# Kernel optimization log

Hardware: AMD Instinct MI355X
Metric: run time of the kernel (lower is better)

The kernel has to match this reference:

```python
import jax, jax.numpy as jnp
import numpy as np

B, T, A, G, E, H = 64, 128, 30, 3, 64, 256
FA, FE, NE = 32, 16, 30
LA = A * 36
SD = A * FA + NE * FE + LA  # 2520


def setup_inputs() -> dict:
    key = jax.random.key(0)
    ks = iter(jax.random.split(key, 64))
    p = lambda *s: jax.random.normal(next(ks), s, jnp.float32) * 0.02
    qvals = jax.random.normal(next(ks), (B, T, A), jnp.float32)
    # ally states with a valid one-hot group type in the last G slots (constant over t)
    ally = jax.random.normal(next(ks), (B, T, A, FA), jnp.float32)
    grp = jax.random.randint(next(ks), (B, A), 0, G)
    onehot = jax.nn.one_hot(grp, G, dtype=jnp.float32)  # (B,A,G)
    ally = ally.at[:, :, :, -G:].set(jnp.broadcast_to(onehot[:, None], (B, T, A, G)))
    rest = jax.random.normal(next(ks), (B, T, NE * FE + LA), jnp.float32)
    states = jnp.concatenate([ally.reshape(B, T, A * FA), rest], axis=2)
    d = {"qvals": qvals, "states": states}
    d["g_w1_W1"] = p(G, SD, H); d["g_w1_b1"] = p(G, H); d["g_w1_W2"] = p(G, H, A * E); d["g_w1_b2"] = p(G, A * E)
    d["g_b1_W1"] = p(G, SD, H); d["g_b1_b1"] = p(G, H); d["g_b1_W2"] = p(G, H, E); d["g_b1_b2"] = p(G, E)
    d["g_w2_W1"] = p(G, SD, H); d["g_w2_b1"] = p(G, H); d["g_w2_W2"] = p(G, H, E); d["g_w2_b2"] = p(G, E)
    d["g_b2_W1"] = p(G, SD, E); d["g_b2_b1"] = p(G, E); d["g_b2_W2"] = p(G, E, 1); d["g_b2_b2"] = p(G, 1)
    d["h_w1_W1"] = p(SD, H); d["h_w1_b1"] = p(H); d["h_w1_W2"] = p(H, G * E); d["h_w1_b2"] = p(G * E)
    d["h_b1_W1"] = p(SD, H); d["h_b1_b1"] = p(H); d["h_b1_W2"] = p(H, E); d["h_b1_b2"] = p(E)
    d["h_w2_W1"] = p(SD, H); d["h_w2_b1"] = p(H); d["h_w2_W2"] = p(H, E); d["h_w2_b2"] = p(E)
    d["h_b2_W1"] = p(SD, E); d["h_b2_b1"] = p(E); d["h_b2_W2"] = p(E, 1); d["h_b2_b2"] = p(1)
    return d


def reference(qvals, states,
              g_w1_W1, g_w1_b1, g_w1_W2, g_w1_b2,
              g_b1_W1, g_b1_b1, g_b1_W2, g_b1_b2,
              g_w2_W1, g_w2_b1, g_w2_W2, g_w2_b2,
              g_b2_W1, g_b2_b1, g_b2_W2, g_b2_b2,
              h_w1_W1, h_w1_b1, h_w1_W2, h_w1_b2,
              h_b1_W1, h_b1_b1, h_b1_W2, h_b1_b2,
              h_w2_W1, h_w2_b1, h_w2_W2, h_w2_b2,
              h_b2_W1, h_b2_b1, h_b2_W2, h_b2_b2):
    N = B * T
    s = states.reshape(N, SD)
    # group masks from the one-hot type slots at t=0 (constant across time)
    ally = states[..., : A * FA].reshape(B, T, A, FA)
    type0 = ally[:, 0, :, -G:]                                  # (B,A,G)
    masks = jnp.transpose(type0 == 1.0, (2, 0, 1)).astype(qvals.dtype)  # (G,B,A)
    mq = (qvals[None] * masks[:, :, None, :]).reshape(G, N, A)  # (G,N,A)

    def gmlp(W1, b1, W2, b2):  # stacked-over-groups 2-layer MLP
        h = jax.nn.relu(jnp.einsum('nd,gdh->gnh', s, W1) + b1[:, None])
        return jnp.einsum('gnh,gho->gno', h, W2) + b2[:, None]

    w1 = jnp.abs(gmlp(g_w1_W1, g_w1_b1, g_w1_W2, g_w1_b2)).reshape(G, N, A, E)
    b1 = gmlp(g_b1_W1, g_b1_b1, g_b1_W2, g_b1_b2)               # (G,N,E)
    w2 = jnp.abs(gmlp(g_w2_W1, g_w2_b1, g_w2_W2, g_w2_b2))      # (G,N,E)
    b2 = gmlp(g_b2_W1, g_b2_b1, g_b2_W2, g_b2_b2)[..., 0]       # (G,N)
    hidden = jax.nn.elu(jnp.einsum('gna,gnae->gne', mq, w1) + b1)
    group_qvals = (jnp.einsum('gne,gne->gn', hidden, w2) + b2).T  # (N,G)

    def hmlp(W1, b1_, W2, b2_):
        return jax.nn.relu(s @ W1 + b1_) @ W2 + b2_

    hw1 = jnp.abs(hmlp(h_w1_W1, h_w1_b1, h_w1_W2, h_w1_b2)).reshape(N, G, E)
    hb1 = hmlp(h_b1_W1, h_b1_b1, h_b1_W2, h_b1_b2)              # (N,E)
    hw2 = jnp.abs(hmlp(h_w2_W1, h_w2_b1, h_w2_W2, h_w2_b2))     # (N,E)
    hb2 = hmlp(h_b2_W1, h_b2_b1, h_b2_W2, h_b2_b2)[:, 0]        # (N,)
    hid = jax.nn.elu(jnp.einsum('ng,nge->ne', group_qvals, hw1) + hb1)
    qtot = jnp.einsum('ne,ne->n', hid, hw2) + hb2
    return qtot.reshape(B, T, 1)
```

## Files before the change

### kernel.cpp

```cpp
#include <hip/hip_runtime.h>

typedef unsigned short u16;
typedef __bf16 bf16x8 __attribute__((ext_vector_type(8)));
typedef float f32x4 __attribute__((ext_vector_type(4)));
typedef unsigned short u16x8 __attribute__((ext_vector_type(8)));

#define NB 64
#define NT 128
#define NA 30
#define NG 3
#define NE 64
#define NH 256
#define NN 8192
#define SD 2520
#define KP 2560
#define NC 3328
#define NKT 40
#define NITER 20

__device__ __forceinline__ u16 f2bf(float f) {
  union { float f; unsigned u; } c; c.f = f;
  unsigned u = c.u + 0x7FFFu + ((c.u >> 16) & 1u);
  return (u16)(u >> 16);
}
__device__ __forceinline__ float bf2f(u16 h) {
  union { unsigned u; float f; } c; c.u = ((unsigned)h) << 16;
  return c.f;
}
__device__ __forceinline__ float eluf(float x) { return x > 0.f ? x : expm1f(x); }

__device__ __forceinline__ void gload16(const u16* g, u16* l) {
  __builtin_amdgcn_global_load_lds((const __attribute__((address_space(1))) void*)g,
                                   (__attribute__((address_space(3))) void*)l, 16, 0, 0);
}

__device__ __forceinline__ float wredsum(float v) {
  #pragma unroll
  for (int d = 32; d > 0; d >>= 1) v += __shfl_xor(v, d, 64);
  return v;
}

__global__ __launch_bounds__(256) void pack_all_k(
    const float* __restrict__ states,
    const float* __restrict__ gw1W1, const float* __restrict__ gw1b1,
    const float* __restrict__ gb1W1, const float* __restrict__ gb1b1,
    const float* __restrict__ gw2W1, const float* __restrict__ gw2b1,
    const float* __restrict__ gb2W1, const float* __restrict__ gb2b1,
    const float* __restrict__ hw1W1, const float* __restrict__ hw1b1,
    const float* __restrict__ hb1W1, const float* __restrict__ hb1b1,
    const float* __restrict__ hw2W1, const float* __restrict__ hw2b1,
    const float* __restrict__ hb2W1, const float* __restrict__ hb2b1,
    const float* __restrict__ gw1W2, const float* __restrict__ gb1W2,
    const float* __restrict__ gw2W2, const float* __restrict__ hw1W2,
    const float* __restrict__ hb1W2, const float* __restrict__ hw2W2,
    u16* __restrict__ A, u16* __restrict__ BT, float* __restrict__ bias,
    u16* __restrict__ w2tw1, u16* __restrict__ w2ts, int* __restrict__ grps) {
  int bid = blockIdx.x;
  if (bid < 10240) {
    int tid = bid * 256 + threadIdx.x;
    int n = tid / 320, kq = tid - n * 320;
    int k = kq * 8;
    u16x8 v;
    if (k < SD) {
      const float4* p = reinterpret_cast<const float4*>(states + (size_t)n * SD + k);
      float4 x0 = p[0], x1 = p[1];
      v[0]=f2bf(x0.x); v[1]=f2bf(x0.y); v[2]=f2bf(x0.z); v[3]=f2bf(x0.w);
      v[4]=f2bf(x1.x); v[5]=f2bf(x1.y); v[6]=f2bf(x1.z); v[7]=f2bf(x1.w);
    } else {
      v[0]=0;v[1]=0;v[2]=0;v[3]=0;v[4]=0;v[5]=0;v[6]=0;v[7]=0;
    }
    *reinterpret_cast<u16x8*>(A + (size_t)n * KP + k) = v;
  } else if (bid < 14400) {
    int tid = (bid - 10240) * 256 + threadIdx.x;
    int kq = tid / NC, j = tid - kq * NC;
    const float* W; const float* bsrc; size_t cbase; int stride; int q;
    if (j < 768)        { q=j;      int g=q>>8; W=gw1W1; cbase=(size_t)g*SD*NH + (q&255); stride=NH; bsrc=gw1b1; }
    else if (j < 1536)  { q=j-768;  int g=q>>8; W=gb1W1; cbase=(size_t)g*SD*NH + (q&255); stride=NH; bsrc=gb1b1; }
    else if (j < 2304)  { q=j-1536; int g=q>>8; W=gw2W1; cbase=(size_t)g*SD*NH + (q&255); stride=NH; bsrc=gw2b1; }
    else if (j < 2496)  { q=j-2304; int g=q>>6; W=gb2W1; cbase=(size_t)g*SD*NE + (q&63);  stride=NE; bsrc=gb2b1; }
    else if (j < 2752)  { q=j-2496; W=hw1W1; cbase=q; stride=NH; bsrc=hw1b1; }
    else if (j < 3008)  { q=j-2752; W=hb1W1; cbase=q; stride=NH; bsrc=hb1b1; }
    else if (j < 3264)  { q=j-3008; W=hw2W1; cbase=q; stride=NH; bsrc=hw2b1; }
    else                { q=j-3264; W=hb2W1; cbase=q; stride=NE; bsrc=hb2b1; }
    int k = kq * 8;
    u16x8 v;
    #pragma unroll
    for (int i = 0; i < 8; ++i) {
      int d = k + i;
      v[i] = (d < SD) ? f2bf(W[cbase + (size_t)d * stride]) : (u16)0;
    }
    *reinterpret_cast<u16x8*>(BT + (size_t)j * KP + k) = v;
    if (kq == 0) bias[j] = bsrc[q];
  } else if (bid < 15120) {
    int tid = (bid - 14400) * 256 + threadIdx.x;
    int lane = tid & 63, cf = (tid >> 6) & 3, ks = (tid >> 8) & 7, slab = tid >> 11;
    int g = slab / 30, a = slab - g * 30;
    int e = cf * 16 + (lane & 15);
    int h0 = ks * 32 + (lane >> 4) * 8;
    const float* src = gw1W2 + (size_t)g * (NH * 1920) + (size_t)h0 * 1920 + a * 64 + e;
    u16x8 v;
    #pragma unroll
    for (int i = 0; i < 8; ++i) v[i] = f2bf(src[(size_t)i * 1920]);
    *reinterpret_cast<u16x8*>(w2tw1 + (size_t)tid * 8) = v;
  } else if (bid < 15208) {
    int tid = (bid - 15120) * 256 + threadIdx.x;
    int lane = tid & 63, cf = (tid >> 6) & 3, ks = (tid >> 8) & 7, u = tid >> 11;
    int e = cf * 16 + (lane & 15);
    int h0 = ks * 32 + (lane >> 4) * 8;
    const float* src; int stride;
    if (u < 3)       { src = gb1W2 + (size_t)u * (NH*NE) + (size_t)h0 * NE + e;     stride = NE; }
    else if (u < 6)  { src = gw2W2 + (size_t)(u-3) * (NH*NE) + (size_t)h0 * NE + e; stride = NE; }
    else if (u < 9)  { src = hw1W2 + (size_t)h0 * (NG*NE) + (u-6)*64 + e;           stride = NG*NE; }
    else if (u == 9) { src = hb1W2 + (size_t)h0 * NE + e;                           stride = NE; }
    else             { src = hw2W2 + (size_t)h0 * NE + e;                           stride = NE; }
    u16x8 v;
    #pragma unroll
    for (int i = 0; i < 8; ++i) v[i] = f2bf(src[(size_t)i * stride]);
    *reinterpret_cast<u16x8*>(w2ts + (size_t)tid * 8) = v;
  } else {
    int b = threadIdx.x;
    if (b >= NB) return;
    int gv0 = 0, gv1 = 0;
    int cnt0 = 0, cnt1 = 0, cnt2 = 0;
    #pragma unroll
    for (int a = 0; a < NA; ++a) {
      int g = 0;
      #pragma unroll
      for (int gi = 0; gi < NG; ++gi)
        if (states[(size_t)b * NT * SD + a * 32 + 29 + gi] == 1.0f) g = gi;
      if (a < 15) gv0 |= g << (2 * a); else gv1 |= g << (2 * (a - 15));
      if (g == 0) ++cnt0; else if (g == 1) ++cnt1; else ++cnt2;
    }
    int off0 = 0, off1 = cnt0, off2 = cnt0 + cnt1;
    #pragma unroll
    for (int a = 0; a < NA; ++a) {
      int g = (a < 15) ? ((gv0 >> (2 * a)) & 3) : ((gv1 >> (2 * (a - 15))) & 3);
      int pos;
      if (g == 0) pos = off0++; else if (g == 1) pos = off1++; else pos = off2++;
      grps[b * NA + pos] = a | (g << 16);
    }
  }
}

__global__ __launch_bounds__(512, 2) void gemm1_k(const u16* __restrict__ A, const u16* __restrict__ BT,
    const float* __restrict__ bias, u16* __restrict__ act) {
  __shared__ u16 lds[65536];
  int t = threadIdx.x;
  int wg = blockIdx.x;
  int swz = (wg & 7) * 52 + (wg >> 3);
  int by = swz / 13, bx = swz - by * 13;
  size_t mb = (size_t)by * 256, nb = (size_t)bx * 256;
  int lane = t & 63, w = t >> 6;
  int wm = (w >> 2) * 128;
  int wn = (w & 3) * 64;
  int l15 = lane & 15, hi = lane >> 4;

  int srow = t >> 3;
  int scol = (((t & 7) ^ (srow & 7)) << 3);
  const u16* aS = A + (mb + srow) * KP + scol;
  const u16* bS = BT + (nb + srow) * KP + scol;

#define STGA(buf, h, kt) { \
    u16* d_ = lds + (buf) * 32768 + (h) * 8192; \
    const u16* s_ = aS + (size_t)((h) * 128) * KP + (size_t)(kt) * 64; \
    gload16(s_,                  d_ + t * 8); \
    gload16(s_ + (size_t)64 * KP, d_ + 4096 + t * 8); }
#define STGB(buf, h, kt) { \
    u16* d_ = lds + (buf) * 32768 + 16384 + (h) * 8192; \
    const u16* s_ = bS + (size_t)((h) * 128) * KP + (size_t)(kt) * 64; \
    gload16(s_,                  d_ + t * 8); \
    gload16(s_ + (size_t)64 * KP, d_ + 4096 + t * 8); }

  f32x4 acc[8][4];
  #pragma unroll
  for (int mi = 0; mi < 8; ++mi)
    #pragma unroll
    for (int ni = 0; ni < 4; ++ni) acc[mi][ni] = {0.f, 0.f, 0.f, 0.f};

  const char* A0 = (const char*)(lds) + (wm ? 16384 : 0);
  const char* B0 = (const char*)(lds) + 32768 + ((wn & 128) ? 16384 : 0);
  const char* A1 = A0 + 65536;
  const char* B1 = B0 + 65536;
  int rx = l15 & 7;
  int aBase = l15 * 128;
  int bBase = ((wn & 64) + l15) * 128;
  int slot0 = (hi ^ rx) << 4;
  int slot1 = ((4 + hi) ^ rx) << 4;

  bf16x8 afA[4][2], afB[4][2], bfA[2][2], bfB[2][2];

#define LD_AFA(Ab) { _Pragma("unroll") for (int m_ = 0; m_ < 4; ++m_) { \
    afA[m_][0] = *reinterpret_cast<const bf16x8*>((Ab) + aBase + m_ * 2048 + slot0); \
    afA[m_][1] = *reinterpret_cast<const bf16x8*>((Ab) + aBase + m_ * 2048 + slot1); } }
#define LD_AFB(Ab) { _Pragma("unroll") for (int m_ = 0; m_ < 4; ++m_) { \
    afB[m_][0] = *reinterpret_cast<const bf16x8*>((Ab) + aBase + (4 + m_) * 2048 + slot0); \
    afB[m_][1] = *reinterpret_cast<const bf16x8*>((Ab) + aBase + (4 + m_) * 2048 + slot1); } }
#define LD_BFA(Bb) { _Pragma("unroll") for (int n_ = 0; n_ < 2; ++n_) { \
    bfA[n_][0] = *reinterpret_cast<const bf16x8*>((Bb) + bBase + n_ * 2048 + slot0); \
    bfA[n_][1] = *reinterpret_cast<const bf16x8*>((Bb) + bBase + n_ * 2048 + slot1); } }
#define LD_BFB(Bb) { _Pragma("unroll") for (int n_ = 0; n_ < 2; ++n_) { \
    bfB[n_][0] = *reinterpret_cast<const bf16x8*>((Bb) + bBase + (2 + n_) * 2048 + slot0); \
    bfB[n_][1] = *reinterpret_cast<const bf16x8*>((Bb) + bBase + (2 + n_) * 2048 + slot1); } }
#define MM_Q(AF, BF, MO, NO) { _Pragma("unroll") for (int m_ = 0; m_ < 4; ++m_) \
    _Pragma("unroll") for (int n_ = 0; n_ < 2; ++n_) { \
      acc[(MO)+m_][(NO)+n_] = __builtin_amdgcn_mfma_f32_16x16x32_bf16(AF[m_][0], BF[n_][0], acc[(MO)+m_][(NO)+n_], 0, 0, 0); \
      acc[(MO)+m_][(NO)+n_] = __builtin_amdgcn_mfma_f32_16x16x32_bf16(AF[m_][1], BF[n_][1], acc[(MO)+m_][(NO)+n_], 0, 0, 0); } }
#define SYNC_IN  __builtin_amdgcn_s_barrier(); \
                 asm volatile("s_waitcnt lgkmcnt(0)" ::: "memory"); \
                 __builtin_amdgcn_sched_barrier(0); \
                 __builtin_amdgcn_s_setprio(1);
#define SYNC_OUT __builtin_amdgcn_s_setprio(0); \
                 __builtin_amdgcn_s_barrier(); \
                 asm volatile("" ::: "memory");

  STGA(0, 0, 0); STGA(0, 1, 0); STGB(0, 0, 0); STGB(0, 1, 0);
  STGB(1, 0, 1); STGB(1, 1, 1);
  asm volatile("s_waitcnt vmcnt(4)" ::: "memory");
  __builtin_amdgcn_s_barrier();
  asm volatile("" ::: "memory");

  for (int it = 0; it < NITER; ++it) {
    int k1 = 2 * it + 1;
    bool t2 = (2 * it + 2 < NKT), t3 = (2 * it + 3 < NKT);
    LD_AFA(A0); LD_BFA(B0);
    STGA(1, 0, k1);
    SYNC_IN; MM_Q(afA, bfA, 0, 0); SYNC_OUT;
    LD_BFB(B0);
    STGA(1, 1, k1);
    SYNC_IN; MM_Q(afA, bfB, 0, 2); SYNC_OUT;
    LD_AFB(A0);
    if (t2) STGB(0, 0, 2 * it + 2);
    SYNC_IN; MM_Q(afB, bfB, 4, 2); SYNC_OUT;
    if (t2) STGB(0, 1, 2 * it + 2);
    __builtin_amdgcn_s_barrier();
    __builtin_amdgcn_s_setprio(1); MM_Q(afB, bfA, 4, 0); __builtin_amdgcn_s_setprio(0);
    if (it == NITER - 1) { asm volatile("s_waitcnt vmcnt(0)" ::: "memory"); }
    else                 { asm volatile("s_waitcnt vmcnt(4)" ::: "memory"); }
    __builtin_amdgcn_s_barrier();
    asm volatile("" ::: "memory");
    LD_AFA(A1); LD_BFA(B1);
    if (t2) STGA(0, 0, 2 * it + 2);
    SYNC_IN; MM_Q(afA, bfA, 0, 0); SYNC_OUT;
    LD_BFB(B1);
    if (t2) STGA(0, 1, 2 * it + 2);
    SYNC_IN; MM_Q(afA, bfB, 0, 2); SYNC_OUT;
    LD_AFB(A1);
    if (t3) STGB(1, 0, 2 * it + 3);
    SYNC_IN; MM_Q(afB, bfB, 4, 2); SYNC_OUT;
    if (t3) STGB(1, 1, 2 * it + 3);
    __builtin_amdgcn_s_barrier();
    __builtin_amdgcn_s_setprio(1); MM_Q(afB, bfA, 4, 0); __builtin_amdgcn_s_setprio(0);
    if (t3) { asm volatile("s_waitcnt vmcnt(4)" ::: "memory"); }
    __builtin_amdgcn_s_barrier();
    asm volatile("" ::: "memory");
  }

  int r00 = (int)mb + wm + hi * 4;
  int cc0 = (int)nb + wn + l15;
  float bv0 = bias[cc0], bv1 = bias[cc0 + 16], bv2 = bias[cc0 + 32], bv3 = bias[cc0 + 48];
  #pragma unroll
  for (int mi = 0; mi < 8; ++mi) {
    #pragma unroll
    for (int i = 0; i < 4; ++i) {
      u16* dst = act + (size_t)(r00 + mi * 16 + i) * NC + cc0;
      float v0 = acc[mi][0][i] + bv0; v0 = v0 > 0.f ? v0 : 0.f;
      float v1 = acc[mi][1][i] + bv1; v1 = v1 > 0.f ? v1 : 0.f;
      float v2 = acc[mi][2][i] + bv2; v2 = v2 > 0.f ? v2 : 0.f;
      float v3 = acc[mi][3][i] + bv3; v3 = v3 > 0.f ? v3 : 0.f;
      dst[0] = f2bf(v0); dst[16] = f2bf(v1); dst[32] = f2bf(v2); dst[48] = f2bf(v3);
    }
  }
#undef STGA
#undef STGB
#undef LD_AFA
#undef LD_AFB
#undef LD_BFA
#undef LD_BFB
#undef MM_Q
#undef SYNC_IN
#undef SYNC_OUT
}

__global__ __launch_bounds__(128) void c1a_k(const u16* __restrict__ act, const float* __restrict__ qvals,
    const int* __restrict__ grps, const u16* __restrict__ w2tw1, const float* __restrict__ gw1b2,
    float* __restrict__ qw1part) {
  int t = threadIdx.x, lane = t & 63, w = t >> 6;
  int rb = blockIdx.x;
  int ch = blockIdx.y;
  int nb0 = rb * 32 + w * 16;
  int b = rb >> 2;
  int l16 = lane & 15, lk8 = (lane >> 4) * 8;
  float g0[4][4], g1[4][4], g2[4][4];
  #pragma unroll
  for (int cf = 0; cf < 4; ++cf)
    #pragma unroll
    for (int i = 0; i < 4; ++i) { g0[cf][i]=0.f; g1[cf][i]=0.f; g2[cf][i]=0.f; }
  const u16* arow = act + (size_t)(nb0 + l16) * NC;
  int r4 = nb0 + (lane >> 4) * 4;
  const int* sl = grps + b * NA + ch * 6;
  int curg = -1;
  bf16x8 af0[4], af1[4];
  for (int ai = 0; ai < 6; ++ai) {
    int ent = sl[ai];
    int a = ent & 0xffff, g = ent >> 16;
    if (g != curg) {
      curg = g;
      const u16* abase = arow + g * NH;
      #pragma unroll
      for (int ks = 0; ks < 4; ++ks) {
        af0[ks] = *reinterpret_cast<const bf16x8*>(abase + ks * 32 + lk8);
        af1[ks] = *reinterpret_cast<const bf16x8*>(abase + (4 + ks) * 32 + lk8);
      }
    }
    f32x4 t4[4], u4[4];
    #pragma unroll
    for (int cf = 0; cf < 4; ++cf) { t4[cf] = {0.f,0.f,0.f,0.f}; u4[cf] = {0.f,0.f,0.f,0.f}; }
    const u16* bbase = w2tw1 + (size_t)(g * NA + a) * 16384 + lane * 8;
    #pragma unroll
    for (int ks = 0; ks < 4; ++ks) {
      #pragma unroll
      for (int cf = 0; cf < 4; ++cf) {
        bf16x8 bf0 = *reinterpret_cast<const bf16x8*>(bbase + (ks * 4 + cf) * 512);
        bf16x8 bf1 = *reinterpret_cast<const bf16x8*>(bbase + ((4 + ks) * 4 + cf) * 512);
        t4[cf] = __builtin_amdgcn_mfma_f32_16x16x32_bf16(af0[ks], bf0, t4[cf], 0, 0, 0);
        u4[cf] = __builtin_amdgcn_mfma_f32_16x16x32_bf16(af1[ks], bf1, u4[cf], 0, 0, 0);
      }
    }
    float qv[4];
    #pragma unroll
    for (int i = 0; i < 4; ++i) qv[i] = qvals[(size_t)(r4 + i) * NA + a];
    const float* bias = gw1b2 + (size_t)g * (NA * NE) + a * NE;
    float vv[4][4];
    #pragma unroll
    for (int cf = 0; cf < 4; ++cf) {
      float bv = bias[cf*16 + l16];
      #pragma unroll
      for (int i = 0; i < 4; ++i) vv[cf][i] = qv[i] * fabsf(t4[cf][i] + u4[cf][i] + bv);
    }
    if (g == 0) {
      #pragma unroll
      for (int cf = 0; cf < 4; ++cf)
        #pragma unroll
        for (int i = 0; i < 4; ++i) g0[cf][i] += vv[cf][i];
    } else if (g == 1) {
      #pragma unroll
      for (int cf = 0; cf < 4; ++cf)
        #pragma unroll
        for (int i = 0; i < 4; ++i) g1[cf][i] += vv[cf][i];
    } else {
      #pragma unroll
      for (int cf = 0; cf < 4; ++cf)
        #pragma unroll
        for (int i = 0; i < 4; ++i) g2[cf][i] += vv[cf][i];
    }
  }
  float* outp = qw1part + (size_t)ch * NN * 192;
  #pragma unroll
  for (int cf = 0; cf < 4; ++cf)
    #pragma unroll
    for (int i = 0; i < 4; ++i) {
      size_t base = (size_t)(r4 + i) * 192 + cf * 16 + l16;
      outp[base]       = g0[cf][i];
      outp[base + 64]  = g1[cf][i];
      outp[base + 128] = g2[cf][i];
    }
}

__global__ __launch_bounds__(256) void c1b_k(const u16* __restrict__ act, const u16* __restrict__ w2ts,
    const float* __restrict__ gb1b2, const float* __restrict__ gw2b2, const float* __restrict__ hw1b2,
    const float* __restrict__ hb1b2, const float* __restrict__ hw2b2,
    float* __restrict__ b1s, float* __restrict__ w2s, float* __restrict__ hw1s,
    float* __restrict__ hb1s, float* __restrict__ hw2s) {
  int u = blockIdx.x, blk = blockIdx.y;
  int t = threadIdx.x, lane = t & 63, w = t >> 6;
  int nb0 = blk * 64 + w * 16;
  int l16 = lane & 15, lk8 = (lane >> 4) * 8;
  int aoff = (u < 3) ? 768 + u * 256 : (u < 6) ? 1536 + (u-3) * 256 : (u < 9) ? 2496 : (u == 9) ? 2752 : 3008;
  const float* bias; float* outp; int ostride; bool ab;
  if (u < 3)       { bias = gb1b2 + u * 64;       outp = b1s  + u * 64;     ostride = 192; ab = false; }
  else if (u < 6)  { bias = gw2b2 + (u-3) * 64;   outp = w2s  + (u-3) * 64; ostride = 192; ab = true; }
  else if (u < 9)  { bias = hw1b2 + (u-6) * 64;   outp = hw1s + (u-6) * 64; ostride = 192; ab = true; }
  else if (u == 9) { bias = hb1b2;                outp = hb1s;              ostride = 64;  ab = false; }
  else             { bias = hw2b2;                outp = hw2s;              ostride = 64;  ab = true; }
  f32x4 t4[4];
  #pragma unroll
  for (int cf = 0; cf < 4; ++cf) t4[cf] = {0.f, 0.f, 0.f, 0.f};
  const u16* arow = act + (size_t)(nb0 + l16) * NC + aoff;
  const u16* bbase = w2ts + (size_t)u * 16384 + lane * 8;
  #pragma unroll
  for (int ks = 0; ks < 8; ++ks) {
    bf16x8 af = *reinterpret_cast<const bf16x8*>(arow + ks * 32 + lk8);
    #pragma unroll
    for (int cf = 0; cf < 4; ++cf) {
      bf16x8 bf = *reinterpret_cast<const bf16x8*>(bbase + (ks * 4 + cf) * 512);
      t4[cf] = __builtin_amdgcn_mfma_f32_16x16x32_bf16(af, bf, t4[cf], 0, 0, 0);
    }
  }
  int r4 = nb0 + (lane >> 4) * 4;
  #pragma unroll
  for (int cf = 0; cf < 4; ++cf) {
    float bv = bias[cf*16 + l16];
    #pragma unroll
    for (int i = 0; i < 4; ++i) {
      float v = t4[cf][i] + bv;
      if (ab) v = fabsf(v);
      outp[(size_t)(r4 + i) * ostride + cf * 16 + l16] = v;
    }
  }
}

__global__ __launch_bounds__(256) void c2_k(const u16* __restrict__ act,
    const float* __restrict__ qw1part, const float* __restrict__ b1s, const float* __restrict__ w2s,
    const float* __restrict__ hw1s, const float* __restrict__ hb1s, const float* __restrict__ hw2s,
    const float* __restrict__ gb2W2, const float* __restrict__ gb2b2,
    const float* __restrict__ hb2W2, const float* __restrict__ hb2b2,
    float* __restrict__ out) {
  int gtid = blockIdx.x * 256 + threadIdx.x;
  int n = gtid >> 6, e = gtid & 63;
  const u16* an = act + (size_t)n * NC;
  float q0 = 0.f, q1 = 0.f, q2 = 0.f;
  #pragma unroll
  for (int ch = 0; ch < 5; ++ch) {
    const float* qp = qw1part + (size_t)ch * NN * 192 + (size_t)n * 192;
    q0 += qp[e]; q1 += qp[64 + e]; q2 += qp[128 + e];
  }
  const float* b1n = b1s + (size_t)n * 192;
  const float* w2n = w2s + (size_t)n * 192;
  float s0 = bf2f(an[2304 + e]) * gb2W2[e]       + eluf(q0 + b1n[e])       * w2n[e];
  float s1 = bf2f(an[2368 + e]) * gb2W2[64 + e]  + eluf(q1 + b1n[64 + e])  * w2n[64 + e];
  float s2 = bf2f(an[2432 + e]) * gb2W2[128 + e] + eluf(q2 + b1n[128 + e]) * w2n[128 + e];
  float sh = bf2f(an[3264 + e]) * hb2W2[e];
  float gq0 = wredsum(s0) + gb2b2[0];
  float gq1 = wredsum(s1) + gb2b2[1];
  float gq2 = wredsum(s2) + gb2b2[2];
  float hb2v = wredsum(sh) + hb2b2[0];
  const float* hw1n = hw1s + (size_t)n * 192;
  float hv = gq0 * hw1n[e] + gq1 * hw1n[64 + e] + gq2 * hw1n[128 + e] + hb1s[(size_t)n * 64 + e];
  float c = eluf(hv) * hw2s[(size_t)n * 64 + e];
  float qt = wredsum(c) + hb2v;
  if (e == 0) out[n] = qt;
}

extern "C" void kernel_launch(void* const* d_in, const int* in_sizes, int n_in,
                              void* d_out, int out_size, void* d_ws, size_t ws_size,
                              hipStream_t stream) {
  const float* qvals  = (const float*)d_in[0];
  const float* states = (const float*)d_in[1];
  const float* gw1W1 = (const float*)d_in[2];
  const float* gw1b1 = (const float*)d_in[3];
  const float* gw1W2 = (const float*)d_in[4];
  const float* gw1b2 = (const float*)d_in[5];
  const float* gb1W1 = (const float*)d_in[6];
  const float* gb1b1 = (const float*)d_in[7];
  const float* gb1W2 = (const float*)d_in[8];
  const float* gb1b2 = (const float*)d_in[9];
  const float* gw2W1 = (const float*)d_in[10];
  const float* gw2b1 = (const float*)d_in[11];
  const float* gw2W2 = (const float*)d_in[12];
  const float* gw2b2 = (const float*)d_in[13];
  const float* gb2W1 = (const float*)d_in[14];
  const float* gb2b1 = (const float*)d_in[15];
  const float* gb2W2 = (const float*)d_in[16];
  const float* gb2b2 = (const float*)d_in[17];
  const float* hw1W1 = (const float*)d_in[18];
  const float* hw1b1 = (const float*)d_in[19];
  const float* hw1W2 = (const float*)d_in[20];
  const float* hw1b2 = (const float*)d_in[21];
  const float* hb1W1 = (const float*)d_in[22];
  const float* hb1b1 = (const float*)d_in[23];
  const float* hb1W2 = (const float*)d_in[24];
  const float* hb1b2 = (const float*)d_in[25];
  const float* hw2W1 = (const float*)d_in[26];
  const float* hw2b1 = (const float*)d_in[27];
  const float* hw2W2 = (const float*)d_in[28];
  const float* hw2b2 = (const float*)d_in[29];
  const float* hb2W1 = (const float*)d_in[30];
  const float* hb2b1 = (const float*)d_in[31];
  const float* hb2W2 = (const float*)d_in[32];
  const float* hb2b2 = (const float*)d_in[33];
  float* out = (float*)d_out;

  char* p = (char*)d_ws;
  u16* A       = (u16*)p;   p += (size_t)NN * KP * 2;
  u16* BT      = (u16*)p;   p += (size_t)NC * KP * 2;
  u16* act     = (u16*)p;   p += (size_t)NN * NC * 2;
  u16* w2tw1   = (u16*)p;   p += (size_t)5760 * NH * 2;
  u16* w2ts    = (u16*)p;   p += (size_t)704 * NH * 2;
  float* bias  = (float*)p; p += (size_t)NC * 4;
  int* grps    = (int*)p;   p += (size_t)NB * NA * 4;
  float* b1s   = (float*)p; p += (size_t)NN * 192 * 4;
  float* w2s   = (float*)p; p += (size_t)NN * 192 * 4;
  float* hw1s  = (float*)p; p += (size_t)NN * 192 * 4;
  float* hb1s  = (float*)p; p += (size_t)NN * 64 * 4;
  float* hw2s  = (float*)p; p += (size_t)NN * 64 * 4;
  float* qw1part = (float*)A;

  pack_all_k<<<15209, 256, 0, stream>>>(states,
                                        gw1W1, gw1b1, gb1W1, gb1b1, gw2W1, gw2b1, gb2W1, gb2b1,
                                        hw1W1, hw1b1, hb1W1, hb1b1, hw2W1, hw2b1, hb2W1, hb2b1,
                                        gw1W2, gb1W2, gw2W2, hw1W2, hb1W2, hw2W2,
                                        A, BT, bias, w2tw1, w2ts, grps);
  gemm1_k<<<416, 512, 0, stream>>>(A, BT, bias, act);
  c1a_k<<<dim3(256, 5), 128, 0, stream>>>(act, qvals, grps, w2tw1, gw1b2, qw1part);
  c1b_k<<<dim3(11, 128), 256, 0, stream>>>(act, w2ts, gb1b2, gw2b2, hw1b2, hb1b2, hw2b2,
                                           b1s, w2s, hw1s, hb1s, hw2s);
  c2_k<<<2048, 256, 0, stream>>>(act, qw1part, b1s, w2s, hw1s, hb1s, hw2s,
                                 gb2W2, gb2b2, hb2W2, hb2b2, out);
}
```

Baseline: 244.4 us.

## Split c1a work by group instead of fixed agent chunks

The agent-mixing kernel now launches one block column per group rather than five fixed six-agent chunks. Each block loads its group's activation fragments once, loops only over that group's agents using per-batch counts written by the pack kernel, and writes a single 64-wide slice of the result. This drops the five-way partial buffers and the reduction over them in c2, and removes the per-agent group branching and the triple accumulators. In exchange the grid has fewer blocks with uneven work, since per-group agent counts vary per batch.

```diff
diff --git a/kernel.cpp b/kernel.cpp
--- a/kernel.cpp
+++ b/kernel.cpp
@@ -54,7 +54,8 @@
     const float* __restrict__ gw2W2, const float* __restrict__ hw1W2,
     const float* __restrict__ hb1W2, const float* __restrict__ hw2W2,
     u16* __restrict__ A, u16* __restrict__ BT, float* __restrict__ bias,
-    u16* __restrict__ w2tw1, u16* __restrict__ w2ts, int* __restrict__ grps) {
+    u16* __restrict__ w2tw1, u16* __restrict__ w2ts,
+    int* __restrict__ grps, int* __restrict__ gcnt) {
   int bid = blockIdx.x;
   if (bid < 10240) {
     int tid = bid * 256 + threadIdx.x;
@@ -131,13 +132,14 @@
       if (a < 15) gv0 |= g << (2 * a); else gv1 |= g << (2 * (a - 15));
       if (g == 0) ++cnt0; else if (g == 1) ++cnt1; else ++cnt2;
     }
+    gcnt[b * 4 + 0] = cnt0; gcnt[b * 4 + 1] = cnt1; gcnt[b * 4 + 2] = cnt2;
     int off0 = 0, off1 = cnt0, off2 = cnt0 + cnt1;
     #pragma unroll
     for (int a = 0; a < NA; ++a) {
       int g = (a < 15) ? ((gv0 >> (2 * a)) & 3) : ((gv1 >> (2 * (a - 15))) & 3);
       int pos;
       if (g == 0) pos = off0++; else if (g == 1) pos = off1++; else pos = off2++;
-      grps[b * NA + pos] = a | (g << 16);
+      grps[b * NA + pos] = a;
     }
   }
 }
@@ -282,36 +284,34 @@
 }
 
 __global__ __launch_bounds__(128) void c1a_k(const u16* __restrict__ act, const float* __restrict__ qvals,
-    const int* __restrict__ grps, const u16* __restrict__ w2tw1, const float* __restrict__ gw1b2,
-    float* __restrict__ qw1part) {
+    const int* __restrict__ grps, const int* __restrict__ gcnt, const u16* __restrict__ w2tw1,
+    const float* __restrict__ gw1b2, float* __restrict__ qw1acc) {
   int t = threadIdx.x, lane = t & 63, w = t >> 6;
   int rb = blockIdx.x;
-  int ch = blockIdx.y;
+  int g = blockIdx.y;
   int nb0 = rb * 32 + w * 16;
   int b = rb >> 2;
   int l16 = lane & 15, lk8 = (lane >> 4) * 8;
-  float g0[4][4], g1[4][4], g2[4][4];
+  int cnt0 = gcnt[b * 4], cnt1 = gcnt[b * 4 + 1], cnt2 = gcnt[b * 4 + 2];
+  int start = (g >= 1 ? cnt0 : 0) + (g >= 2 ? cnt1 : 0);
+  int cnt = (g == 0) ? cnt0 : (g == 1) ? cnt1 : cnt2;
+  float gacc[4][4];
   #pragma unroll
   for (int cf = 0; cf < 4; ++cf)
     #pragma unroll
-    for (int i = 0; i < 4; ++i) { g0[cf][i]=0.f; g1[cf][i]=0.f; g2[cf][i]=0.f; }
+    for (int i = 0; i < 4; ++i) gacc[cf][i] = 0.f;
   const u16* arow = act + (size_t)(nb0 + l16) * NC;
   int r4 = nb0 + (lane >> 4) * 4;
-  const int* sl = grps + b * NA + ch * 6;
-  int curg = -1;
+  const u16* abase = arow + g * NH;
   bf16x8 af0[4], af1[4];
-  for (int ai = 0; ai < 6; ++ai) {
-    int ent = sl[ai];
-    int a = ent & 0xffff, g = ent >> 16;
-    if (g != curg) {
-      curg = g;
-      const u16* abase = arow + g * NH;
-      #pragma unroll
-      for (int ks = 0; ks < 4; ++ks) {
-        af0[ks] = *reinterpret_cast<const bf16x8*>(abase + ks * 32 + lk8);
-        af1[ks] = *reinterpret_cast<const bf16x8*>(abase + (4 + ks) * 32 + lk8);
-      }
-    }
+  #pragma unroll
+  for (int ks = 0; ks < 4; ++ks) {
+    af0[ks] = *reinterpret_cast<const bf16x8*>(abase + ks * 32 + lk8);
+    af1[ks] = *reinterpret_cast<const bf16x8*>(abase + (4 + ks) * 32 + lk8);
+  }
+  const int* sl = grps + b * NA + start;
+  for (int ai = 0; ai < cnt; ++ai) {
+    int a = sl[ai];
     f32x4 t4[4], u4[4];
     #pragma unroll
     for (int cf = 0; cf < 4; ++cf) { t4[cf] = {0.f,0.f,0.f,0.f}; u4[cf] = {0.f,0.f,0.f,0.f}; }
@@ -330,40 +330,18 @@
     #pragma unroll
     for (int i = 0; i < 4; ++i) qv[i] = qvals[(size_t)(r4 + i) * NA + a];
     const float* bias = gw1b2 + (size_t)g * (NA * NE) + a * NE;
-    float vv[4][4];
     #pragma unroll
     for (int cf = 0; cf < 4; ++cf) {
       float bv = bias[cf*16 + l16];
       #pragma unroll
-      for (int i = 0; i < 4; ++i) vv[cf][i] = qv[i] * fabsf(t4[cf][i] + u4[cf][i] + bv);
-    }
-    if (g == 0) {
-      #pragma unroll
-      for (int cf = 0; cf < 4; ++cf)
-        #pragma unroll
-        for (int i = 0; i < 4; ++i) g0[cf][i] += vv[cf][i];
-    } else if (g == 1) {
-      #pragma unroll
-      for (int cf = 0; cf < 4; ++cf)
-        #pragma unroll
-        for (int i = 0; i < 4; ++i) g1[cf][i] += vv[cf][i];
-    } else {
-      #pragma unroll
-      for (int cf = 0; cf < 4; ++cf)
-        #pragma unroll
-        for (int i = 0; i < 4; ++i) g2[cf][i] += vv[cf][i];
-    }
-  }
-  float* outp = qw1part + (size_t)ch * NN * 192;
+      for (int i = 0; i < 4; ++i) gacc[cf][i] += qv[i] * fabsf(t4[cf][i] + u4[cf][i] + bv);
+    }
+  }
   #pragma unroll
   for (int cf = 0; cf < 4; ++cf)
     #pragma unroll
-    for (int i = 0; i < 4; ++i) {
-      size_t base = (size_t)(r4 + i) * 192 + cf * 16 + l16;
-      outp[base]       = g0[cf][i];
-      outp[base + 64]  = g1[cf][i];
-      outp[base + 128] = g2[cf][i];
-    }
+    for (int i = 0; i < 4; ++i)
+      qw1acc[(size_t)(r4 + i) * 192 + g * 64 + cf * 16 + l16] = gacc[cf][i];
 }
 
 __global__ __launch_bounds__(256) void c1b_k(const u16* __restrict__ act, const u16* __restrict__ w2ts,
@@ -410,7 +388,7 @@
 }
 
 __global__ __launch_bounds__(256) void c2_k(const u16* __restrict__ act,
-    const float* __restrict__ qw1part, const float* __restrict__ b1s, const float* __restrict__ w2s,
+    const float* __restrict__ qw1acc, const float* __restrict__ b1s, const float* __restrict__ w2s,
     const float* __restrict__ hw1s, const float* __restrict__ hb1s, const float* __restrict__ hw2s,
     const float* __restrict__ gb2W2, const float* __restrict__ gb2b2,
     const float* __restrict__ hb2W2, const float* __restrict__ hb2b2,
@@ -418,12 +396,8 @@
   int gtid = blockIdx.x * 256 + threadIdx.x;
   int n = gtid >> 6, e = gtid & 63;
   const u16* an = act + (size_t)n * NC;
-  float q0 = 0.f, q1 = 0.f, q2 = 0.f;
-  #pragma unroll
-  for (int ch = 0; ch < 5; ++ch) {
-    const float* qp = qw1part + (size_t)ch * NN * 192 + (size_t)n * 192;
-    q0 += qp[e]; q1 += qp[64 + e]; q2 += qp[128 + e];
-  }
+  const float* qn = qw1acc + (size_t)n * 192;
+  float q0 = qn[e], q1 = qn[64 + e], q2 = qn[128 + e];
   const float* b1n = b1s + (size_t)n * 192;
   const float* w2n = w2s + (size_t)n * 192;
   float s0 = bf2f(an[2304 + e]) * gb2W2[e]       + eluf(q0 + b1n[e])       * w2n[e];
@@ -488,22 +462,23 @@
   u16* w2ts    = (u16*)p;   p += (size_t)704 * NH * 2;
   float* bias  = (float*)p; p += (size_t)NC * 4;
   int* grps    = (int*)p;   p += (size_t)NB * NA * 4;
+  int* gcnt    = (int*)p;   p += (size_t)NB * 4 * 4;
   float* b1s   = (float*)p; p += (size_t)NN * 192 * 4;
   float* w2s   = (float*)p; p += (size_t)NN * 192 * 4;
   float* hw1s  = (float*)p; p += (size_t)NN * 192 * 4;
   float* hb1s  = (float*)p; p += (size_t)NN * 64 * 4;
   float* hw2s  = (float*)p; p += (size_t)NN * 64 * 4;
-  float* qw1part = (float*)A;
+  float* qw1acc = (float*)A;
 
   pack_all_k<<<15209, 256, 0, stream>>>(states,
                                         gw1W1, gw1b1, gb1W1, gb1b1, gw2W1, gw2b1, gb2W1, gb2b1,
                                         hw1W1, hw1b1, hb1W1, hb1b1, hw2W1, hw2b1, hb2W1, hb2b1,
                                         gw1W2, gb1W2, gw2W2, hw1W2, hb1W2, hw2W2,
-                                        A, BT, bias, w2tw1, w2ts, grps);
+                                        A, BT, bias, w2tw1, w2ts, grps, gcnt);
   gemm1_k<<<416, 512, 0, stream>>>(A, BT, bias, act);
-  c1a_k<<<dim3(256, 5), 128, 0, stream>>>(act, qvals, grps, w2tw1, gw1b2, qw1part);
+  c1a_k<<<dim3(256, 3), 128, 0, stream>>>(act, qvals, grps, gcnt, w2tw1, gw1b2, qw1acc);
   c1b_k<<<dim3(11, 128), 256, 0, stream>>>(act, w2ts, gb1b2, gw2b2, hw1b2, hb1b2, hw2b2,
                                            b1s, w2s, hw1s, hb1s, hw2s);
-  c2_k<<<2048, 256, 0, stream>>>(act, qw1part, b1s, w2s, hw1s, hb1s, hw2s,
+  c2_k<<<2048, 256, 0, stream>>>(act, qw1acc, b1s, w2s, hw1s, hb1s, hw2s,
                                  gb2W2, gb2b2, hb2W2, hb2b2, out);
 }
```

Result: faster. 237.2 us (median of 2 runs) (-3.0%).
